# Kernel optimization log

Measured on AMD Instinct MI355X. Metric: run time of the kernel, lower is better.

Reference implementation:

```python
import jax, jax.numpy as jnp
import numpy as np

B, D, H, W, C = 4, 8, 16, 16, 512
K_RED = 8
R = C // K_RED          # reduced channels for Q/K
EPS = 1e-3              # keras LayerNormalization default epsilon


def setup_inputs() -> dict:
    key = jax.random.key(0)
    ks = jax.random.split(key, 8)
    s = 0.02
    f32 = jnp.float32
    return {
        "x":  jax.random.normal(ks[0], (B, D, H, W, C), f32),
        # 1x1x1 Conv3D == per-position linear over channels
        "wq": (jax.random.normal(ks[1], (C, R), f32) * s), "bq": jnp.zeros((R,), f32),
        "wk": (jax.random.normal(ks[2], (C, R), f32) * s), "bk": jnp.zeros((R,), f32),
        "wv": (jax.random.normal(ks[3], (C, C), f32) * s), "bv": jnp.zeros((C,), f32),
        "wm": (jax.random.normal(ks[4], (C, C), f32) * s), "bm": jnp.zeros((C,), f32),
        "g1": jnp.ones((C,), f32), "b1": jnp.zeros((C,), f32),
        "g2": jnp.ones((C,), f32), "b2": jnp.zeros((C,), f32),
    }


def _layer_norm(x, g, b):
    m = jnp.mean(x, axis=-1, keepdims=True)
    v = jnp.mean(jnp.square(x - m), axis=-1, keepdims=True)
    return (x - m) * jax.lax.rsqrt(v + EPS) * g + b


def reference(x, wq, bq, wk, bk, wv, bv, wm, bm, g1, b1, g2, b2):
    b, d, h, w, c = x.shape
    f = h * w
    xf = x.reshape(b, d, f, c)                      # [B,D,F,C]
    Q = xf @ wq + bq                                # [B,D,F,R]
    K = xf @ wk + bk                                # [B,D,F,R]
    V = xf @ wv + bv                                # [B,D,F,C]
    # full global scores: [B, D, F, D, F]
    e = jnp.einsum('bifr,bgjr->bifgj', Q, K)
    alphas = jax.nn.softmax(e.reshape(b, d, f, d * f), axis=-1)
    alphas = alphas.reshape(b, d, f, d, f)
    # original einsum 'bdfgh,bdhi->bdfi' sums over key-depth g and uses V at
    # the query depth d; fold the g-sum first, then per-depth F x F matmul.
    a2 = alphas.sum(axis=3)                         # [B,D,F,F]
    attn = jnp.einsum('bdfh,bdhc->bdfc', a2, V)     # [B,D,F,C]
    y1 = _layer_norm(attn + xf, g1, b1)
    y2 = _layer_norm(y1 + jax.nn.relu(y1 @ wm + bm), g2, b2)
    return y2.reshape(b, d, h, w, c)
```

## Files before the change

### kernel.cpp

```cpp
#include <hip/hip_runtime.h>
#include <cstdint>

#define LN_EPS 1e-3f
using u16 = unsigned short;
using u32 = unsigned int;
typedef __attribute__((ext_vector_type(8))) short bh8;
typedef __attribute__((ext_vector_type(4))) float f4;
#define MFMA16(A,B,C) __builtin_amdgcn_mfma_f32_16x16x32_bf16((A),(B),(C),0,0,0)

__device__ __forceinline__ u16 bf16r(float f){
    union{float f;u32 u;} c; c.f=f;
    return (u16)((c.u + 0x7fffu + ((c.u>>16)&1u))>>16);
}
__device__ __forceinline__ u32 pk2(float a, float b){
    return (u32)bf16r(a) | ((u32)bf16r(b)<<16);
}
__device__ __forceinline__ void glds16(const void* g, void* l){
    __builtin_amdgcn_global_load_lds(
        (const __attribute__((address_space(1))) u32*)g,
        (__attribute__((address_space(3))) u32*)l, 16, 0, 0);
}

__global__ __launch_bounds__(256) void k0_prep(
    const float* __restrict__ x,  const float* __restrict__ wq, const float* __restrict__ wk,
    const float* __restrict__ wv, const float* __restrict__ wm,
    u16* __restrict__ x_pB, u16* __restrict__ wv_p, u16* __restrict__ wm_p, u16* __restrict__ wqk_p)
{
    const int t = threadIdx.x;
    const int c = t & 15, qn = t >> 4;
    const int quad = qn & 3, ntl = qn >> 2;
    const int blk = blockIdx.x;
    if (blk < 256){
        const int bd = blk >> 3, s = blk & 7;
        const float* src = x + ((size_t)(bd*256 + s*32 + quad*8))*512;
        u16* dst = x_pB + (size_t)(bd*8+s)*16384;
        #pragma unroll
        for (int i=0;i<8;++i){
            int nt = i*4 + ntl, n = nt*16 + c;
            float v[8];
            #pragma unroll
            for (int j=0;j<8;++j) v[j] = src[(size_t)j*512 + n];
            uint4 o; o.x=pk2(v[0],v[1]); o.y=pk2(v[2],v[3]); o.z=pk2(v[4],v[5]); o.w=pk2(v[6],v[7]);
            *(uint4*)&dst[((nt*4+quad)*16 + c)*8] = o;
        }
    } else if (blk < 288){
        const int ism = (blk >= 272);
        const int s = ism ? (blk-272) : (blk-256);
        const float* src = (ism ? wm : wv) + (size_t)(s*32 + quad*8)*512;
        u16* dst = (ism ? wm_p : wv_p) + (size_t)s*16384;
        #pragma unroll
        for (int i=0;i<8;++i){
            int nt = i*4 + ntl, n = nt*16 + c;
            float v[8];
            #pragma unroll
            for (int j=0;j<8;++j) v[j] = src[(size_t)j*512 + n];
            uint4 o; o.x=pk2(v[0],v[1]); o.y=pk2(v[2],v[3]); o.z=pk2(v[4],v[5]); o.w=pk2(v[6],v[7]);
            *(uint4*)&dst[((nt*4+quad)*16 + c)*8] = o;
        }
    } else {
        const int s = blk - 288;
        u16* dst = wqk_p + (size_t)s*4096;
        #pragma unroll
        for (int i=0;i<2;++i){
            int nt = i*4 + ntl, n = nt*16 + c;
            const float* src = (n < 64) ? (wq + (size_t)(s*32 + quad*8)*64 + n)
                                        : (wk + (size_t)(s*32 + quad*8)*64 + (n-64));
            float v[8];
            #pragma unroll
            for (int j=0;j<8;++j) v[j] = src[(size_t)j*64];
            uint4 o; o.x=pk2(v[0],v[1]); o.y=pk2(v[2],v[3]); o.z=pk2(v[4],v[5]); o.w=pk2(v[6],v[7]);
            *(uint4*)&dst[((nt*4+quad)*16 + c)*8] = o;
        }
    }
}

__global__ __launch_bounds__(256) void k1_qk(
    const float* __restrict__ x, const float* __restrict__ bq, const float* __restrict__ bk,
    const u16* __restrict__ wqk_p, u16* __restrict__ Qb, u16* __restrict__ Kb)
{
    __shared__ u16 Asf[8192];
    __shared__ u16 Bsf[4096];
    const int t = threadIdx.x, w = t>>6, lane = t&63, quad = lane>>4, c = lane&15;
    const int rowbase = blockIdx.x << 4;
    #pragma unroll
    for (int i=0;i<8;++i){
        int idx = t + (i<<8);
        int fr = idx >> 7, fc4 = idx & 127;
        float4 xv = *(const float4*)&x[(size_t)(rowbase+fr)*512 + fc4*4];
        uint2 pkv; pkv.x = pk2(xv.x,xv.y); pkv.y = pk2(xv.z,xv.w);
        int s = fc4 >> 3, qd = (fc4 >> 1) & 3, j0 = (fc4 & 1)*4;
        *(uint2*)&Asf[s*512 + (qd*16 + fr)*8 + j0] = pkv;
    }
    f4 acc[2] = { {0.f,0.f,0.f,0.f}, {0.f,0.f,0.f,0.f} };
    for (int s=0;s<16;++s){
        __syncthreads();
        #pragma unroll
        for (int i=0;i<2;++i)
            glds16((const char*)wqk_p + (size_t)s*8192 + (w*2+i)*1024 + lane*16,
                   (char*)Bsf + (w*2+i)*1024);
        __syncthreads();
        bh8 a = *(const bh8*)&Asf[s*512 + (quad*16+c)*8];
        #pragma unroll
        for (int nt=0;nt<2;++nt){
            bh8 b = *(const bh8*)&Bsf[(w*2+nt)*512 + (quad*16+c)*8];
            acc[nt] = MFMA16(a, b, acc[nt]);
        }
    }
    const int rt = blockIdx.x;
    #pragma unroll
    for (int nt=0;nt<2;++nt){
        int cqk = w*32 + nt*16 + c;
        bool isQ = (cqk < 64);
        int r = isQ ? cqk : (cqk - 64);
        float bias = isQ ? bq[r] : bk[r];
        int kh = r>>5, q2 = (r>>3)&3, j = r&7;
        u16* dstb = (isQ ? Qb : Kb) + (size_t)((rt*2 + kh)*4 + q2)*128 + j;
        #pragma unroll
        for (int reg=0;reg<4;++reg){
            int cp = quad*4 + reg;
            dstb[cp*8] = bf16r(acc[nt][reg] + bias);
        }
    }
}

__global__ __launch_bounds__(256) void k234(
    const u16* __restrict__ Qb, const u16* __restrict__ Kb,
    const u16* __restrict__ x_pB, const u16* __restrict__ wv_p, const u16* __restrict__ wm_p,
    const float* __restrict__ x, const float* __restrict__ bv,
    const float* __restrict__ g1, const float* __restrict__ b1,
    const float* __restrict__ bm, const float* __restrict__ g2, const float* __restrict__ b2,
    float* __restrict__ out)
{
    __shared__ u16 Bs[16384];
    __shared__ u16 zf[8192];
    __shared__ u16 a2f[4096];
    __shared__ u16 qsf[1024];
    __shared__ float redA[4][16], redB[4][16];
    const int t = threadIdx.x, w = t>>6, lane = t&63, quad = lane>>4, c = lane&15;
    const int b = blockIdx.x >> 7, rem = blockIdx.x & 127, d = rem >> 4, ft = rem & 15;
    const int bd = b*8 + d, rowbase = (bd<<8) + (ft<<4), rt = rowbase >> 4;
    const char* Kbase = (const char*)Kb + (size_t)b*262144;
    const char* xpb   = (const char*)x_pB + (size_t)bd*262144;

    if (w < 2) glds16((const char*)Qb + (size_t)rt*2048 + w*1024 + lane*16, (char*)qsf + w*1024);
    __syncthreads();
    bh8 aq0 = *(const bh8*)&qsf[(quad*16+c)*8];
    bh8 aq1 = *(const bh8*)&qsf[512 + (quad*16+c)*8];

    float lp[4] = {0.f,0.f,0.f,0.f};
    float a2r[4][2][2];
    #pragma unroll
    for (int r=0;r<4;++r){ a2r[r][0][0]=0.f; a2r[r][0][1]=0.f; a2r[r][1][0]=0.f; a2r[r][1][1]=0.f; }

    for (int cc=0; cc<16; ++cc){
        if (cc) __syncthreads();
        #pragma unroll
        for (int i=0;i<4;++i)
            glds16(Kbase + (size_t)cc*16384 + (w*4+i)*1024 + lane*16, (char*)Bs + (w*4+i)*1024);
        __syncthreads();
        f4 sa[2] = { {0.f,0.f,0.f,0.f}, {0.f,0.f,0.f,0.f} };
        #pragma unroll
        for (int kt=0;kt<2;++kt){
            bh8 b0 = *(const bh8*)&Bs[(w*2+kt)*1024 +       (quad*16+c)*8];
            bh8 b1v= *(const bh8*)&Bs[(w*2+kt)*1024 + 512 + (quad*16+c)*8];
            sa[kt] = MFMA16(aq0, b0, sa[kt]);
            sa[kt] = MFMA16(aq1, b1v, sa[kt]);
        }
        const int h = cc & 1;
        #pragma unroll
        for (int kt=0;kt<2;++kt)
            #pragma unroll
            for (int reg=0;reg<4;++reg){
                float e = __expf(sa[kt][reg]);
                lp[reg] += e;
                a2r[reg][h][kt] += e;
            }
    }
    #pragma unroll
    for (int reg=0;reg<4;++reg){
        float v = lp[reg];
        v += __shfl_xor(v,1,64); v += __shfl_xor(v,2,64);
        v += __shfl_xor(v,4,64); v += __shfl_xor(v,8,64);
        lp[reg] = v;
    }
    if (c==0){
        #pragma unroll
        for (int reg=0;reg<4;++reg) redA[w][quad*4+reg] = lp[reg];
    }
    __syncthreads();
    float fac[4];
    #pragma unroll
    for (int reg=0;reg<4;++reg){
        int q = quad*4+reg;
        fac[reg] = 1.f/(redA[0][q]+redA[1][q]+redA[2][q]+redA[3][q]);
    }
    #pragma unroll
    for (int reg=0;reg<4;++reg){
        int q = quad*4+reg;
        #pragma unroll
        for (int h=0;h<2;++h)
            #pragma unroll
            for (int kt=0;kt<2;++kt){
                int j = h*128 + (w*2+kt)*16 + c;
                a2f[(j>>5)*512 + (((j>>3)&3)*16 + q)*8 + (j&7)] = bf16r(a2r[reg][h][kt]*fac[reg]);
            }
    }
    __syncthreads();

    f4 zacc[8];
    #pragma unroll
    for (int nt=0;nt<8;++nt) zacc[nt] = (f4){0.f,0.f,0.f,0.f};
    for (int s=0;s<8;++s){
        if (s) __syncthreads();
        #pragma unroll
        for (int i=0;i<8;++i)
            glds16(xpb + (size_t)s*32768 + (w*8+i)*1024 + lane*16, (char*)Bs + (w*8+i)*1024);
        __syncthreads();
        bh8 a = *(const bh8*)&a2f[s*512 + (quad*16+c)*8];
        #pragma unroll
        for (int nt=0;nt<8;++nt){
            bh8 bb = *(const bh8*)&Bs[((w*8+nt)*4 + quad)*128 + c*8];
            zacc[nt] = MFMA16(a, bb, zacc[nt]);
        }
    }
    __syncthreads();
    #pragma unroll
    for (int nt=0;nt<8;++nt)
        #pragma unroll
        for (int reg=0;reg<4;++reg){
            int col = w*128 + nt*16 + c;
            zf[(col>>5)*512 + (((col>>3)&3)*16 + quad*4+reg)*8 + (col&7)] = bf16r(zacc[nt][reg]);
        }
    __syncthreads();

    f4 cacc[8];
    #pragma unroll
    for (int nt=0;nt<8;++nt) cacc[nt] = (f4){0.f,0.f,0.f,0.f};
    for (int s=0;s<16;++s){
        if (s) __syncthreads();
        #pragma unroll
        for (int i=0;i<8;++i)
            glds16((const char*)wv_p + (size_t)s*32768 + (w*8+i)*1024 + lane*16, (char*)Bs + (w*8+i)*1024);
        __syncthreads();
        bh8 a = *(const bh8*)&zf[s*512 + (quad*16+c)*8];
        #pragma unroll
        for (int nt=0;nt<8;++nt){
            bh8 bb = *(const bh8*)&Bs[((w*8+nt)*4 + quad)*128 + c*8];
            cacc[nt] = MFMA16(a, bb, cacc[nt]);
        }
    }
    {
        float sv[4] = {0.f,0.f,0.f,0.f}, qv2[4] = {0.f,0.f,0.f,0.f};
        #pragma unroll
        for (int nt=0;nt<8;++nt){
            int col = w*128 + nt*16 + c;
            float bvv = bv[col];
            #pragma unroll
            for (int reg=0;reg<4;++reg){
                int row = rowbase + quad*4 + reg;
                float val = cacc[nt][reg] + bvv + x[(size_t)row*512 + col];
                cacc[nt][reg] = val;
                sv[reg] += val; qv2[reg] = fmaf(val,val,qv2[reg]);
            }
        }
        #pragma unroll
        for (int reg=0;reg<4;++reg){
            float s1=sv[reg], s2=qv2[reg];
            s1 += __shfl_xor(s1,1,64); s2 += __shfl_xor(s2,1,64);
            s1 += __shfl_xor(s1,2,64); s2 += __shfl_xor(s2,2,64);
            s1 += __shfl_xor(s1,4,64); s2 += __shfl_xor(s2,4,64);
            s1 += __shfl_xor(s1,8,64); s2 += __shfl_xor(s2,8,64);
            sv[reg]=s1; qv2[reg]=s2;
        }
        if (c==0){
            #pragma unroll
            for (int reg=0;reg<4;++reg){ redA[w][quad*4+reg]=sv[reg]; redB[w][quad*4+reg]=qv2[reg]; }
        }
        __syncthreads();
        float mean[4], rstd[4];
        #pragma unroll
        for (int reg=0;reg<4;++reg){
            int q = quad*4+reg;
            float S  = redA[0][q]+redA[1][q]+redA[2][q]+redA[3][q];
            float Q2 = redB[0][q]+redB[1][q]+redB[2][q]+redB[3][q];
            float m = S*(1.f/512.f);
            float var = Q2*(1.f/512.f) - m*m;
            mean[reg]=m; rstd[reg]=rsqrtf(var + LN_EPS);
        }
        #pragma unroll
        for (int nt=0;nt<8;++nt){
            int col = w*128 + nt*16 + c;
            float gg = g1[col], bb1 = b1[col];
            #pragma unroll
            for (int reg=0;reg<4;++reg){
                float y = (cacc[nt][reg]-mean[reg])*rstd[reg]*gg + bb1;
                cacc[nt][reg] = y;
                zf[(col>>5)*512 + (((col>>3)&3)*16 + quad*4+reg)*8 + (col&7)] = bf16r(y);
            }
        }
        __syncthreads();
    }

    f4 dacc[8];
    #pragma unroll
    for (int nt=0;nt<8;++nt) dacc[nt] = (f4){0.f,0.f,0.f,0.f};
    for (int s=0;s<16;++s){
        if (s) __syncthreads();
        #pragma unroll
        for (int i=0;i<8;++i)
            glds16((const char*)wm_p + (size_t)s*32768 + (w*8+i)*1024 + lane*16, (char*)Bs + (w*8+i)*1024);
        __syncthreads();
        bh8 a = *(const bh8*)&zf[s*512 + (quad*16+c)*8];
        #pragma unroll
        for (int nt=0;nt<8;++nt){
            bh8 bb = *(const bh8*)&Bs[((w*8+nt)*4 + quad)*128 + c*8];
            dacc[nt] = MFMA16(a, bb, dacc[nt]);
        }
    }
    {
        float sv[4] = {0.f,0.f,0.f,0.f}, qv2[4] = {0.f,0.f,0.f,0.f};
        #pragma unroll
        for (int nt=0;nt<8;++nt){
            int col = w*128 + nt*16 + c;
            float bmv = bm[col];
            #pragma unroll
            for (int reg=0;reg<4;++reg){
                float hh = fmaxf(dacc[nt][reg]+bmv, 0.f) + cacc[nt][reg];
                dacc[nt][reg] = hh;
                sv[reg] += hh; qv2[reg] = fmaf(hh,hh,qv2[reg]);
            }
        }
        #pragma unroll
        for (int reg=0;reg<4;++reg){
            float s1=sv[reg], s2=qv2[reg];
            s1 += __shfl_xor(s1,1,64); s2 += __shfl_xor(s2,1,64);
            s1 += __shfl_xor(s1,2,64); s2 += __shfl_xor(s2,2,64);
            s1 += __shfl_xor(s1,4,64); s2 += __shfl_xor(s2,4,64);
            s1 += __shfl_xor(s1,8,64); s2 += __shfl_xor(s2,8,64);
            sv[reg]=s1; qv2[reg]=s2;
        }
        __syncthreads();
        if (c==0){
            #pragma unroll
            for (int reg=0;reg<4;++reg){ redA[w][quad*4+reg]=sv[reg]; redB[w][quad*4+reg]=qv2[reg]; }
        }
        __syncthreads();
        float mean[4], rstd[4];
        #pragma unroll
        for (int reg=0;reg<4;++reg){
            int q = quad*4+reg;
            float S  = redA[0][q]+redA[1][q]+redA[2][q]+redA[3][q];
            float Q2 = redB[0][q]+redB[1][q]+redB[2][q]+redB[3][q];
            float m = S*(1.f/512.f);
            float var = Q2*(1.f/512.f) - m*m;
            mean[reg]=m; rstd[reg]=rsqrtf(var + LN_EPS);
        }
        #pragma unroll
        for (int nt=0;nt<8;++nt){
            int col = w*128 + nt*16 + c;
            float gg = g2[col], bb2 = b2[col];
            #pragma unroll
            for (int reg=0;reg<4;++reg){
                int row = rowbase + quad*4 + reg;
                out[(size_t)row*512 + col] = (dacc[nt][reg]-mean[reg])*rstd[reg]*gg + bb2;
            }
        }
    }
}

extern "C" void kernel_launch(void* const* d_in, const int* in_sizes, int n_in,
                              void* d_out, int out_size, void* d_ws, size_t ws_size,
                              hipStream_t stream) {
    (void)in_sizes; (void)n_in; (void)out_size; (void)ws_size;
    const float* x  = (const float*)d_in[0];
    const float* wq = (const float*)d_in[1];
    const float* bq = (const float*)d_in[2];
    const float* wk = (const float*)d_in[3];
    const float* bk = (const float*)d_in[4];
    const float* wv = (const float*)d_in[5];
    const float* bv = (const float*)d_in[6];
    const float* wm = (const float*)d_in[7];
    const float* bm = (const float*)d_in[8];
    const float* g1 = (const float*)d_in[9];
    const float* b1 = (const float*)d_in[10];
    const float* g2 = (const float*)d_in[11];
    const float* b2 = (const float*)d_in[12];

    u16* x_pB  = (u16*)d_ws;
    u16* wv_p  = x_pB + (size_t)4194304;
    u16* wm_p  = wv_p + 262144;
    u16* wqk_p = wm_p + 262144;
    u16* Qb    = wqk_p + 65536;
    u16* Kb    = Qb + 524288;
    float* outp = (float*)d_out;

    k0_prep<<<304, 256, 0, stream>>>(x, wq, wk, wv, wm, x_pB, wv_p, wm_p, wqk_p);
    k1_qk  <<<512, 256, 0, stream>>>(x, bq, bk, wqk_p, Qb, Kb);
    k234   <<<512, 256, 0, stream>>>(Qb, Kb, x_pB, wv_p, wm_p, x, bv, g1, b1, bm, g2, b2, outp);
}
```

Baseline: 153.0 us.

## Precompute V with fused QKV projection and reassociate attention matmul

The V projection moves into the Q/K projection kernel, which now computes Q, K and V together from one bf16 x tile. The attention step multiplies the attention weights directly by the precomputed V, replacing the old (a2 @ x) @ Wv chain in which each of the D depth slices redid the full C×C projection. Blocks grow to 512 threads covering 32 rows, and every stage's weight and K loads are double-buffered in LDS so the next tile loads while the current one computes. The costs are an extra V buffer in global memory, more LDS per block, and fewer blocks, which may lower occupancy.

```diff
diff --git a/kernel.cpp b/kernel.cpp
--- a/kernel.cpp
+++ b/kernel.cpp
@@ -22,159 +22,188 @@
 }
 
 __global__ __launch_bounds__(256) void k0_prep(
-    const float* __restrict__ x,  const float* __restrict__ wq, const float* __restrict__ wk,
+    const float* __restrict__ wq, const float* __restrict__ wk,
     const float* __restrict__ wv, const float* __restrict__ wm,
-    u16* __restrict__ x_pB, u16* __restrict__ wv_p, u16* __restrict__ wm_p, u16* __restrict__ wqk_p)
+    u16* __restrict__ wqkv_p, u16* __restrict__ wm_p)
 {
     const int t = threadIdx.x;
     const int c = t & 15, qn = t >> 4;
     const int quad = qn & 3, ntl = qn >> 2;
     const int blk = blockIdx.x;
-    if (blk < 256){
-        const int bd = blk >> 3, s = blk & 7;
-        const float* src = x + ((size_t)(bd*256 + s*32 + quad*8))*512;
-        u16* dst = x_pB + (size_t)(bd*8+s)*16384;
-        #pragma unroll
-        for (int i=0;i<8;++i){
-            int nt = i*4 + ntl, n = nt*16 + c;
+    if (blk < 32){
+        const int s = blk >> 1, hh = blk & 1;
+        const int krow = s*32 + quad*8;
+        u16* dst = wqkv_p + (size_t)s*20480;
+        #pragma unroll
+        for (int i=0;i<5;++i){
+            const int nt = hh*20 + i*4 + ntl;
+            const int n = nt*16 + c;
+            const float* src; int ldw;
+            if (n < 64){ src = wq + (size_t)krow*64 + n; ldw = 64; }
+            else if (n < 128){ src = wk + (size_t)krow*64 + (n-64); ldw = 64; }
+            else { src = wv + (size_t)krow*512 + (n-128); ldw = 512; }
             float v[8];
             #pragma unroll
-            for (int j=0;j<8;++j) v[j] = src[(size_t)j*512 + n];
+            for (int j=0;j<8;++j) v[j] = src[(size_t)j*ldw];
             uint4 o; o.x=pk2(v[0],v[1]); o.y=pk2(v[2],v[3]); o.z=pk2(v[4],v[5]); o.w=pk2(v[6],v[7]);
             *(uint4*)&dst[((nt*4+quad)*16 + c)*8] = o;
         }
-    } else if (blk < 288){
-        const int ism = (blk >= 272);
-        const int s = ism ? (blk-272) : (blk-256);
-        const float* src = (ism ? wm : wv) + (size_t)(s*32 + quad*8)*512;
-        u16* dst = (ism ? wm_p : wv_p) + (size_t)s*16384;
-        #pragma unroll
-        for (int i=0;i<8;++i){
-            int nt = i*4 + ntl, n = nt*16 + c;
+    } else {
+        const int bb = blk - 32;
+        const int s = bb >> 1, hh = bb & 1;
+        const int krow = s*32 + quad*8;
+        u16* dst = wm_p + (size_t)s*16384;
+        #pragma unroll
+        for (int i=0;i<4;++i){
+            const int nt = hh*16 + i*4 + ntl;
+            const int n = nt*16 + c;
+            const float* src = wm + (size_t)krow*512 + n;
             float v[8];
             #pragma unroll
-            for (int j=0;j<8;++j) v[j] = src[(size_t)j*512 + n];
+            for (int j=0;j<8;++j) v[j] = src[(size_t)j*512];
             uint4 o; o.x=pk2(v[0],v[1]); o.y=pk2(v[2],v[3]); o.z=pk2(v[4],v[5]); o.w=pk2(v[6],v[7]);
             *(uint4*)&dst[((nt*4+quad)*16 + c)*8] = o;
         }
-    } else {
-        const int s = blk - 288;
-        u16* dst = wqk_p + (size_t)s*4096;
-        #pragma unroll
-        for (int i=0;i<2;++i){
-            int nt = i*4 + ntl, n = nt*16 + c;
-            const float* src = (n < 64) ? (wq + (size_t)(s*32 + quad*8)*64 + n)
-                                        : (wk + (size_t)(s*32 + quad*8)*64 + (n-64));
-            float v[8];
-            #pragma unroll
-            for (int j=0;j<8;++j) v[j] = src[(size_t)j*64];
-            uint4 o; o.x=pk2(v[0],v[1]); o.y=pk2(v[2],v[3]); o.z=pk2(v[4],v[5]); o.w=pk2(v[6],v[7]);
-            *(uint4*)&dst[((nt*4+quad)*16 + c)*8] = o;
-        }
-    }
-}
-
-__global__ __launch_bounds__(256) void k1_qk(
+    }
+}
+
+__global__ __launch_bounds__(512) void k1_qkv(
     const float* __restrict__ x, const float* __restrict__ bq, const float* __restrict__ bk,
-    const u16* __restrict__ wqk_p, u16* __restrict__ Qb, u16* __restrict__ Kb)
+    const u16* __restrict__ wqkv_p,
+    u16* __restrict__ Qb, u16* __restrict__ Kb, u16* __restrict__ Vb)
 {
-    __shared__ u16 Asf[8192];
-    __shared__ u16 Bsf[4096];
-    const int t = threadIdx.x, w = t>>6, lane = t&63, quad = lane>>4, c = lane&15;
-    const int rowbase = blockIdx.x << 4;
+    __shared__ u16 Asf[16384];
+    __shared__ u16 Bs[2][20480];
+    const int t = threadIdx.x, w = t>>6, lane = t&63, quad = (lane>>4)&3, c = lane&15;
+    const int rg = w>>2, cg = w&3;
+    const int rowbase = blockIdx.x << 5;
+
     #pragma unroll
     for (int i=0;i<8;++i){
-        int idx = t + (i<<8);
-        int fr = idx >> 7, fc4 = idx & 127;
+        const int idx = t + (i<<9);
+        const int fr = idx >> 7, fc4 = idx & 127;
         float4 xv = *(const float4*)&x[(size_t)(rowbase+fr)*512 + fc4*4];
         uint2 pkv; pkv.x = pk2(xv.x,xv.y); pkv.y = pk2(xv.z,xv.w);
-        int s = fc4 >> 3, qd = (fc4 >> 1) & 3, j0 = (fc4 & 1)*4;
-        *(uint2*)&Asf[s*512 + (qd*16 + fr)*8 + j0] = pkv;
-    }
-    f4 acc[2] = { {0.f,0.f,0.f,0.f}, {0.f,0.f,0.f,0.f} };
+        const int s = fc4 >> 3, qd = (fc4 >> 1) & 3, j0 = (fc4 & 1)*4;
+        *(uint2*)&Asf[(fr>>4)*8192 + s*512 + (qd*16 + (fr&15))*8 + j0] = pkv;
+    }
+    f4 acc[10];
+    #pragma unroll
+    for (int i=0;i<10;++i) acc[i] = (f4){0.f,0.f,0.f,0.f};
+    #pragma unroll
+    for (int i=0;i<5;++i)
+        glds16((const char*)wqkv_p + (size_t)w*5120 + i*1024 + lane*16,
+               (char*)Bs[0] + w*5120 + i*1024);
+    __syncthreads();
+
     for (int s=0;s<16;++s){
-        __syncthreads();
-        #pragma unroll
-        for (int i=0;i<2;++i)
-            glds16((const char*)wqk_p + (size_t)s*8192 + (w*2+i)*1024 + lane*16,
-                   (char*)Bsf + (w*2+i)*1024);
-        __syncthreads();
-        bh8 a = *(const bh8*)&Asf[s*512 + (quad*16+c)*8];
-        #pragma unroll
-        for (int nt=0;nt<2;++nt){
-            bh8 b = *(const bh8*)&Bsf[(w*2+nt)*512 + (quad*16+c)*8];
-            acc[nt] = MFMA16(a, b, acc[nt]);
-        }
-    }
-    const int rt = blockIdx.x;
-    #pragma unroll
-    for (int nt=0;nt<2;++nt){
-        int cqk = w*32 + nt*16 + c;
-        bool isQ = (cqk < 64);
-        int r = isQ ? cqk : (cqk - 64);
-        float bias = isQ ? bq[r] : bk[r];
-        int kh = r>>5, q2 = (r>>3)&3, j = r&7;
-        u16* dstb = (isQ ? Qb : Kb) + (size_t)((rt*2 + kh)*4 + q2)*128 + j;
-        #pragma unroll
-        for (int reg=0;reg<4;++reg){
-            int cp = quad*4 + reg;
-            dstb[cp*8] = bf16r(acc[nt][reg] + bias);
-        }
-    }
-}
-
-__global__ __launch_bounds__(256) void k234(
-    const u16* __restrict__ Qb, const u16* __restrict__ Kb,
-    const u16* __restrict__ x_pB, const u16* __restrict__ wv_p, const u16* __restrict__ wm_p,
+        const u16* Bcur = Bs[s&1];
+        if (s+1 < 16){
+            #pragma unroll
+            for (int i=0;i<5;++i)
+                glds16((const char*)wqkv_p + (size_t)(s+1)*40960 + (size_t)w*5120 + i*1024 + lane*16,
+                       (char*)Bs[(s+1)&1] + w*5120 + i*1024);
+        }
+        bh8 a = *(const bh8*)&Asf[rg*8192 + s*512 + (quad*16+c)*8];
+        #pragma unroll
+        for (int nt2=0;nt2<10;++nt2){
+            bh8 bb = *(const bh8*)&Bcur[((cg*10+nt2)*4 + quad)*128 + c*8];
+            acc[nt2] = MFMA16(a, bb, acc[nt2]);
+        }
+        __syncthreads();
+    }
+
+    const int rt = (blockIdx.x<<1) + rg;
+    const int bd = rowbase >> 8;
+    const int kloc = (rowbase & 255) + rg*16 + quad*4;
+    const int sv = kloc >> 5, kq = (kloc >> 3) & 3, jk0 = kloc & 7;
+    #pragma unroll
+    for (int nt2=0;nt2<10;++nt2){
+        const int colb = cg*160 + nt2*16;
+        if (colb < 128){
+            const bool isK = (colb >= 64);
+            const int r = colb - (isK ? 64 : 0) + c;
+            const float bias = isK ? bk[r] : bq[r];
+            u16* dstb = (isK ? Kb : Qb) + ((size_t)(rt*2 + (r>>5))*4 + ((r>>3)&3))*128 + (r&7);
+            #pragma unroll
+            for (int reg=0;reg<4;++reg)
+                dstb[(quad*4+reg)*8] = bf16r(acc[nt2][reg] + bias);
+        } else {
+            const int ntv = (colb - 128) >> 4;
+            u16* dstv = Vb + (size_t)bd*131072 + (size_t)sv*16384
+                           + (size_t)((ntv*4+kq)*128 + c*8 + jk0);
+            ushort4 o;
+            o.x = bf16r(acc[nt2][0]); o.y = bf16r(acc[nt2][1]);
+            o.z = bf16r(acc[nt2][2]); o.w = bf16r(acc[nt2][3]);
+            *(ushort4*)dstv = o;
+        }
+    }
+}
+
+__global__ __launch_bounds__(512) void k234(
+    const u16* __restrict__ Qb, const u16* __restrict__ Kb, const u16* __restrict__ Vb,
+    const u16* __restrict__ wm_p,
     const float* __restrict__ x, const float* __restrict__ bv,
     const float* __restrict__ g1, const float* __restrict__ b1,
     const float* __restrict__ bm, const float* __restrict__ g2, const float* __restrict__ b2,
     float* __restrict__ out)
 {
-    __shared__ u16 Bs[16384];
-    __shared__ u16 zf[8192];
-    __shared__ u16 a2f[4096];
-    __shared__ u16 qsf[1024];
-    __shared__ float redA[4][16], redB[4][16];
-    const int t = threadIdx.x, w = t>>6, lane = t&63, quad = lane>>4, c = lane&15;
-    const int b = blockIdx.x >> 7, rem = blockIdx.x & 127, d = rem >> 4, ft = rem & 15;
-    const int bd = b*8 + d, rowbase = (bd<<8) + (ft<<4), rt = rowbase >> 4;
+    __shared__ u16 Bs[2][16384];
+    __shared__ u16 y1f[16384];
+    __shared__ u16 a2f[8192];
+    __shared__ u16 qsf[2048];
+    __shared__ float redA[2][4][16], redB[2][4][16];
+    const int t = threadIdx.x, w = t>>6, lane = t&63, quad = (lane>>4)&3, c = lane&15;
+    const int rg = w>>2, cg = w&3;
+    const int bd = blockIdx.x & 31, ftile = blockIdx.x >> 5;
+    const int b = bd >> 3;
+    const int rowbase = (bd<<8) + (ftile<<5);
+    const int rt00 = rowbase >> 4;
     const char* Kbase = (const char*)Kb + (size_t)b*262144;
-    const char* xpb   = (const char*)x_pB + (size_t)bd*262144;
-
-    if (w < 2) glds16((const char*)Qb + (size_t)rt*2048 + w*1024 + lane*16, (char*)qsf + w*1024);
+    const char* Vbase = (const char*)Vb + (size_t)bd*262144;
+
+    if (w < 4) glds16((const char*)Qb + (size_t)rt00*2048 + w*1024 + lane*16,
+                      (char*)qsf + w*1024);
+    #pragma unroll
+    for (int i=0;i<2;++i)
+        glds16(Kbase + (size_t)w*2048 + i*1024 + lane*16, (char*)Bs[0] + w*2048 + i*1024);
     __syncthreads();
-    bh8 aq0 = *(const bh8*)&qsf[(quad*16+c)*8];
-    bh8 aq1 = *(const bh8*)&qsf[512 + (quad*16+c)*8];
+    bh8 aq0 = *(const bh8*)&qsf[rg*1024 + (quad*16+c)*8];
+    bh8 aq1 = *(const bh8*)&qsf[rg*1024 + 512 + (quad*16+c)*8];
 
     float lp[4] = {0.f,0.f,0.f,0.f};
-    float a2r[4][2][2];
-    #pragma unroll
-    for (int r=0;r<4;++r){ a2r[r][0][0]=0.f; a2r[r][0][1]=0.f; a2r[r][1][0]=0.f; a2r[r][1][1]=0.f; }
-
+    float a2r[4][2][2] = {};
+    #pragma unroll
     for (int cc=0; cc<16; ++cc){
-        if (cc) __syncthreads();
-        #pragma unroll
-        for (int i=0;i<4;++i)
-            glds16(Kbase + (size_t)cc*16384 + (w*4+i)*1024 + lane*16, (char*)Bs + (w*4+i)*1024);
-        __syncthreads();
-        f4 sa[2] = { {0.f,0.f,0.f,0.f}, {0.f,0.f,0.f,0.f} };
+        const u16* Bcur = Bs[cc&1];
+        if (cc+1 < 16){
+            #pragma unroll
+            for (int i=0;i<2;++i)
+                glds16(Kbase + (size_t)(cc+1)*16384 + (size_t)w*2048 + i*1024 + lane*16,
+                       (char*)Bs[(cc+1)&1] + w*2048 + i*1024);
+        }
+        f4 sa[2] = { (f4){0.f,0.f,0.f,0.f}, (f4){0.f,0.f,0.f,0.f} };
         #pragma unroll
         for (int kt=0;kt<2;++kt){
-            bh8 b0 = *(const bh8*)&Bs[(w*2+kt)*1024 +       (quad*16+c)*8];
-            bh8 b1v= *(const bh8*)&Bs[(w*2+kt)*1024 + 512 + (quad*16+c)*8];
+            bh8 b0 = *(const bh8*)&Bcur[(cg*2+kt)*1024 + (quad*16+c)*8];
+            bh8 b1v= *(const bh8*)&Bcur[(cg*2+kt)*1024 + 512 + (quad*16+c)*8];
             sa[kt] = MFMA16(aq0, b0, sa[kt]);
             sa[kt] = MFMA16(aq1, b1v, sa[kt]);
         }
-        const int h = cc & 1;
         #pragma unroll
         for (int kt=0;kt<2;++kt)
             #pragma unroll
             for (int reg=0;reg<4;++reg){
                 float e = __expf(sa[kt][reg]);
                 lp[reg] += e;
-                a2r[reg][h][kt] += e;
-            }
+                a2r[reg][cc&1][kt] += e;
+            }
+        __syncthreads();
+    }
+    {
+        #pragma unroll
+        for (int i=0;i<4;++i)
+            glds16(Vbase + (size_t)w*4096 + i*1024 + lane*16, (char*)Bs[0] + w*4096 + i*1024);
     }
     #pragma unroll
     for (int reg=0;reg<4;++reg){
@@ -185,184 +214,166 @@
     }
     if (c==0){
         #pragma unroll
-        for (int reg=0;reg<4;++reg) redA[w][quad*4+reg] = lp[reg];
+        for (int reg=0;reg<4;++reg) redA[rg][cg][quad*4+reg] = lp[reg];
     }
     __syncthreads();
     float fac[4];
     #pragma unroll
     for (int reg=0;reg<4;++reg){
-        int q = quad*4+reg;
-        fac[reg] = 1.f/(redA[0][q]+redA[1][q]+redA[2][q]+redA[3][q]);
-    }
-    #pragma unroll
-    for (int reg=0;reg<4;++reg){
-        int q = quad*4+reg;
+        const int q = quad*4+reg;
+        fac[reg] = 1.f/(redA[rg][0][q]+redA[rg][1][q]+redA[rg][2][q]+redA[rg][3][q]);
+    }
+    #pragma unroll
+    for (int reg=0;reg<4;++reg)
         #pragma unroll
         for (int h=0;h<2;++h)
             #pragma unroll
             for (int kt=0;kt<2;++kt){
-                int j = h*128 + (w*2+kt)*16 + c;
-                a2f[(j>>5)*512 + (((j>>3)&3)*16 + q)*8 + (j&7)] = bf16r(a2r[reg][h][kt]*fac[reg]);
-            }
-    }
+                const int jp = h*128 + cg*32 + kt*16 + c;
+                a2f[rg*4096 + (jp>>5)*512 + (((jp>>3)&3)*16 + quad*4+reg)*8 + (jp&7)]
+                    = bf16r(a2r[reg][h][kt]*fac[reg]);
+            }
     __syncthreads();
 
-    f4 zacc[8];
-    #pragma unroll
-    for (int nt=0;nt<8;++nt) zacc[nt] = (f4){0.f,0.f,0.f,0.f};
-    for (int s=0;s<8;++s){
-        if (s) __syncthreads();
-        #pragma unroll
-        for (int i=0;i<8;++i)
-            glds16(xpb + (size_t)s*32768 + (w*8+i)*1024 + lane*16, (char*)Bs + (w*8+i)*1024);
-        __syncthreads();
-        bh8 a = *(const bh8*)&a2f[s*512 + (quad*16+c)*8];
-        #pragma unroll
-        for (int nt=0;nt<8;++nt){
-            bh8 bb = *(const bh8*)&Bs[((w*8+nt)*4 + quad)*128 + c*8];
-            zacc[nt] = MFMA16(a, bb, zacc[nt]);
-        }
-    }
-    __syncthreads();
-    #pragma unroll
-    for (int nt=0;nt<8;++nt)
+    f4 cacc[8];
+    #pragma unroll
+    for (int i=0;i<8;++i) cacc[i] = (f4){0.f,0.f,0.f,0.f};
+    for (int s8=0;s8<8;++s8){
+        const u16* Bcur = Bs[s8&1];
+        if (s8+1 < 8){
+            #pragma unroll
+            for (int i=0;i<4;++i)
+                glds16(Vbase + (size_t)(s8+1)*32768 + (size_t)w*4096 + i*1024 + lane*16,
+                       (char*)Bs[(s8+1)&1] + w*4096 + i*1024);
+        }
+        bh8 a = *(const bh8*)&a2f[rg*4096 + s8*512 + (quad*16+c)*8];
+        #pragma unroll
+        for (int nt2=0;nt2<8;++nt2){
+            bh8 bb = *(const bh8*)&Bcur[((cg*8+nt2)*4 + quad)*128 + c*8];
+            cacc[nt2] = MFMA16(a, bb, cacc[nt2]);
+        }
+        __syncthreads();
+    }
+
+    {
+        float sv4[4] = {0.f,0.f,0.f,0.f}, qv2[4] = {0.f,0.f,0.f,0.f};
+        #pragma unroll
+        for (int nt2=0;nt2<8;++nt2){
+            const int col = cg*128 + nt2*16 + c;
+            const float bvv = bv[col];
+            #pragma unroll
+            for (int reg=0;reg<4;++reg){
+                const int row = rowbase + rg*16 + quad*4 + reg;
+                float val = cacc[nt2][reg] + bvv + x[(size_t)row*512 + col];
+                cacc[nt2][reg] = val;
+                sv4[reg] += val; qv2[reg] = fmaf(val,val,qv2[reg]);
+            }
+        }
         #pragma unroll
         for (int reg=0;reg<4;++reg){
-            int col = w*128 + nt*16 + c;
-            zf[(col>>5)*512 + (((col>>3)&3)*16 + quad*4+reg)*8 + (col&7)] = bf16r(zacc[nt][reg]);
-        }
-    __syncthreads();
-
-    f4 cacc[8];
-    #pragma unroll
-    for (int nt=0;nt<8;++nt) cacc[nt] = (f4){0.f,0.f,0.f,0.f};
-    for (int s=0;s<16;++s){
-        if (s) __syncthreads();
-        #pragma unroll
-        for (int i=0;i<8;++i)
-            glds16((const char*)wv_p + (size_t)s*32768 + (w*8+i)*1024 + lane*16, (char*)Bs + (w*8+i)*1024);
-        __syncthreads();
-        bh8 a = *(const bh8*)&zf[s*512 + (quad*16+c)*8];
-        #pragma unroll
-        for (int nt=0;nt<8;++nt){
-            bh8 bb = *(const bh8*)&Bs[((w*8+nt)*4 + quad)*128 + c*8];
-            cacc[nt] = MFMA16(a, bb, cacc[nt]);
-        }
-    }
-    {
-        float sv[4] = {0.f,0.f,0.f,0.f}, qv2[4] = {0.f,0.f,0.f,0.f};
-        #pragma unroll
-        for (int nt=0;nt<8;++nt){
-            int col = w*128 + nt*16 + c;
-            float bvv = bv[col];
-            #pragma unroll
-            for (int reg=0;reg<4;++reg){
-                int row = rowbase + quad*4 + reg;
-                float val = cacc[nt][reg] + bvv + x[(size_t)row*512 + col];
-                cacc[nt][reg] = val;
-                sv[reg] += val; qv2[reg] = fmaf(val,val,qv2[reg]);
-            }
-        }
-        #pragma unroll
-        for (int reg=0;reg<4;++reg){
-            float s1=sv[reg], s2=qv2[reg];
+            float s1=sv4[reg], s2=qv2[reg];
             s1 += __shfl_xor(s1,1,64); s2 += __shfl_xor(s2,1,64);
             s1 += __shfl_xor(s1,2,64); s2 += __shfl_xor(s2,2,64);
             s1 += __shfl_xor(s1,4,64); s2 += __shfl_xor(s2,4,64);
             s1 += __shfl_xor(s1,8,64); s2 += __shfl_xor(s2,8,64);
-            sv[reg]=s1; qv2[reg]=s2;
+            sv4[reg]=s1; qv2[reg]=s2;
         }
         if (c==0){
             #pragma unroll
-            for (int reg=0;reg<4;++reg){ redA[w][quad*4+reg]=sv[reg]; redB[w][quad*4+reg]=qv2[reg]; }
+            for (int reg=0;reg<4;++reg){ redA[rg][cg][quad*4+reg]=sv4[reg]; redB[rg][cg][quad*4+reg]=qv2[reg]; }
         }
         __syncthreads();
         float mean[4], rstd[4];
         #pragma unroll
         for (int reg=0;reg<4;++reg){
-            int q = quad*4+reg;
-            float S  = redA[0][q]+redA[1][q]+redA[2][q]+redA[3][q];
-            float Q2 = redB[0][q]+redB[1][q]+redB[2][q]+redB[3][q];
-            float m = S*(1.f/512.f);
-            float var = Q2*(1.f/512.f) - m*m;
-            mean[reg]=m; rstd[reg]=rsqrtf(var + LN_EPS);
-        }
-        #pragma unroll
-        for (int nt=0;nt<8;++nt){
-            int col = w*128 + nt*16 + c;
-            float gg = g1[col], bb1 = b1[col];
+            const int q = quad*4+reg;
+            const float S  = redA[rg][0][q]+redA[rg][1][q]+redA[rg][2][q]+redA[rg][3][q];
+            const float Q2 = redB[rg][0][q]+redB[rg][1][q]+redB[rg][2][q]+redB[rg][3][q];
+            const float m = S*(1.f/512.f);
+            mean[reg]=m; rstd[reg]=rsqrtf(Q2*(1.f/512.f) - m*m + LN_EPS);
+        }
+        #pragma unroll
+        for (int nt2=0;nt2<8;++nt2){
+            const int col = cg*128 + nt2*16 + c;
+            const float gg = g1[col], bb1 = b1[col];
             #pragma unroll
             for (int reg=0;reg<4;++reg){
-                float y = (cacc[nt][reg]-mean[reg])*rstd[reg]*gg + bb1;
-                cacc[nt][reg] = y;
-                zf[(col>>5)*512 + (((col>>3)&3)*16 + quad*4+reg)*8 + (col&7)] = bf16r(y);
-            }
-        }
+                float y = (cacc[nt2][reg]-mean[reg])*rstd[reg]*gg + bb1;
+                cacc[nt2][reg] = y;
+                y1f[rg*8192 + (col>>5)*512 + (((col>>3)&3)*16 + quad*4+reg)*8 + (col&7)] = bf16r(y);
+            }
+        }
+        #pragma unroll
+        for (int i=0;i<4;++i)
+            glds16((const char*)wm_p + (size_t)w*4096 + i*1024 + lane*16,
+                   (char*)Bs[0] + w*4096 + i*1024);
         __syncthreads();
     }
 
     f4 dacc[8];
     #pragma unroll
-    for (int nt=0;nt<8;++nt) dacc[nt] = (f4){0.f,0.f,0.f,0.f};
+    for (int i=0;i<8;++i) dacc[i] = (f4){0.f,0.f,0.f,0.f};
     for (int s=0;s<16;++s){
-        if (s) __syncthreads();
-        #pragma unroll
-        for (int i=0;i<8;++i)
-            glds16((const char*)wm_p + (size_t)s*32768 + (w*8+i)*1024 + lane*16, (char*)Bs + (w*8+i)*1024);
-        __syncthreads();
-        bh8 a = *(const bh8*)&zf[s*512 + (quad*16+c)*8];
-        #pragma unroll
-        for (int nt=0;nt<8;++nt){
-            bh8 bb = *(const bh8*)&Bs[((w*8+nt)*4 + quad)*128 + c*8];
-            dacc[nt] = MFMA16(a, bb, dacc[nt]);
-        }
-    }
+        const u16* Bcur = Bs[s&1];
+        if (s+1 < 16){
+            #pragma unroll
+            for (int i=0;i<4;++i)
+                glds16((const char*)wm_p + (size_t)(s+1)*32768 + (size_t)w*4096 + i*1024 + lane*16,
+                       (char*)Bs[(s+1)&1] + w*4096 + i*1024);
+        }
+        bh8 a = *(const bh8*)&y1f[rg*8192 + s*512 + (quad*16+c)*8];
+        #pragma unroll
+        for (int nt2=0;nt2<8;++nt2){
+            bh8 bb = *(const bh8*)&Bcur[((cg*8+nt2)*4 + quad)*128 + c*8];
+            dacc[nt2] = MFMA16(a, bb, dacc[nt2]);
+        }
+        __syncthreads();
+    }
+
     {
-        float sv[4] = {0.f,0.f,0.f,0.f}, qv2[4] = {0.f,0.f,0.f,0.f};
-        #pragma unroll
-        for (int nt=0;nt<8;++nt){
-            int col = w*128 + nt*16 + c;
-            float bmv = bm[col];
+        float sv4[4] = {0.f,0.f,0.f,0.f}, qv2[4] = {0.f,0.f,0.f,0.f};
+        #pragma unroll
+        for (int nt2=0;nt2<8;++nt2){
+            const int col = cg*128 + nt2*16 + c;
+            const float bmv = bm[col];
             #pragma unroll
             for (int reg=0;reg<4;++reg){
-                float hh = fmaxf(dacc[nt][reg]+bmv, 0.f) + cacc[nt][reg];
-                dacc[nt][reg] = hh;
-                sv[reg] += hh; qv2[reg] = fmaf(hh,hh,qv2[reg]);
+                float hh = fmaxf(dacc[nt2][reg]+bmv, 0.f) + cacc[nt2][reg];
+                dacc[nt2][reg] = hh;
+                sv4[reg] += hh; qv2[reg] = fmaf(hh,hh,qv2[reg]);
             }
         }
         #pragma unroll
         for (int reg=0;reg<4;++reg){
-            float s1=sv[reg], s2=qv2[reg];
+            float s1=sv4[reg], s2=qv2[reg];
             s1 += __shfl_xor(s1,1,64); s2 += __shfl_xor(s2,1,64);
             s1 += __shfl_xor(s1,2,64); s2 += __shfl_xor(s2,2,64);
             s1 += __shfl_xor(s1,4,64); s2 += __shfl_xor(s2,4,64);
             s1 += __shfl_xor(s1,8,64); s2 += __shfl_xor(s2,8,64);
-            sv[reg]=s1; qv2[reg]=s2;
-        }
-        __syncthreads();
+            sv4[reg]=s1; qv2[reg]=s2;
+        }
         if (c==0){
             #pragma unroll
-            for (int reg=0;reg<4;++reg){ redA[w][quad*4+reg]=sv[reg]; redB[w][quad*4+reg]=qv2[reg]; }
+            for (int reg=0;reg<4;++reg){ redA[rg][cg][quad*4+reg]=sv4[reg]; redB[rg][cg][quad*4+reg]=qv2[reg]; }
         }
         __syncthreads();
         float mean[4], rstd[4];
         #pragma unroll
         for (int reg=0;reg<4;++reg){
-            int q = quad*4+reg;
-            float S  = redA[0][q]+redA[1][q]+redA[2][q]+redA[3][q];
-            float Q2 = redB[0][q]+redB[1][q]+redB[2][q]+redB[3][q];
-            float m = S*(1.f/512.f);
-            float var = Q2*(1.f/512.f) - m*m;
-            mean[reg]=m; rstd[reg]=rsqrtf(var + LN_EPS);
-        }
-        #pragma unroll
-        for (int nt=0;nt<8;++nt){
-            int col = w*128 + nt*16 + c;
-            float gg = g2[col], bb2 = b2[col];
+            const int q = quad*4+reg;
+            const float S  = redA[rg][0][q]+redA[rg][1][q]+redA[rg][2][q]+redA[rg][3][q];
+            const float Q2 = redB[rg][0][q]+redB[rg][1][q]+redB[rg][2][q]+redB[rg][3][q];
+            const float m = S*(1.f/512.f);
+            mean[reg]=m; rstd[reg]=rsqrtf(Q2*(1.f/512.f) - m*m + LN_EPS);
+        }
+        #pragma unroll
+        for (int nt2=0;nt2<8;++nt2){
+            const int col = cg*128 + nt2*16 + c;
+            const float gg = g2[col], bb2 = b2[col];
             #pragma unroll
             for (int reg=0;reg<4;++reg){
-                int row = rowbase + quad*4 + reg;
-                out[(size_t)row*512 + col] = (dacc[nt][reg]-mean[reg])*rstd[reg]*gg + bb2;
+                const int row = rowbase + rg*16 + quad*4 + reg;
+                out[(size_t)row*512 + col] = (dacc[nt2][reg]-mean[reg])*rstd[reg]*gg + bb2;
             }
         }
     }
@@ -386,15 +397,14 @@
     const float* g2 = (const float*)d_in[11];
     const float* b2 = (const float*)d_in[12];
 
-    u16* x_pB  = (u16*)d_ws;
-    u16* wv_p  = x_pB + (size_t)4194304;
-    u16* wm_p  = wv_p + 262144;
-    u16* wqk_p = wm_p + 262144;
-    u16* Qb    = wqk_p + 65536;
-    u16* Kb    = Qb + 524288;
+    u16* wqkv_p = (u16*)d_ws;
+    u16* wm_p   = wqkv_p + 327680;
+    u16* Qb     = wm_p   + 262144;
+    u16* Kb     = Qb     + 524288;
+    u16* Vb     = Kb     + 524288;
     float* outp = (float*)d_out;
 
-    k0_prep<<<304, 256, 0, stream>>>(x, wq, wk, wv, wm, x_pB, wv_p, wm_p, wqk_p);
-    k1_qk  <<<512, 256, 0, stream>>>(x, bq, bk, wqk_p, Qb, Kb);
-    k234   <<<512, 256, 0, stream>>>(Qb, Kb, x_pB, wv_p, wm_p, x, bv, g1, b1, bm, g2, b2, outp);
-}
+    k0_prep<<<64, 256, 0, stream>>>(wq, wk, wv, wm, wqkv_p, wm_p);
+    k1_qkv <<<256, 512, 0, stream>>>(x, bq, bk, wqkv_p, Qb, Kb, Vb);
+    k234   <<<256, 512, 0, stream>>>(Qb, Kb, Vb, wm_p, x, bv, g1, b1, bm, g2, b2, outp);
+}
```

Result: no change. 152.6 us (-0.2%).
